# Performance work log

Hardware: AMD Instinct MI355X
Metric: run time of the kernel (lower is better)

The kernel has to match this reference:

```python
import jax, jax.numpy as jnp
import numpy as np

H = 1024      # hidden_size
NH = 16       # num heads
HD = H // NH  # head dim
B, S = 2, 2048


def setup_inputs() -> dict:
    key = jax.random.key(0)
    ks = jax.random.split(key, 10)
    s = 1.0 / np.sqrt(H)
    return {
        "hidden_states": jax.random.normal(ks[0], (B, S, H), dtype=jnp.float32),
        "attention_mask": jax.random.randint(ks[1], (B, S), 0, 2, dtype=jnp.int32),
        "Wq": jax.random.normal(ks[2], (H, H), dtype=jnp.float32) * s,
        "bq": jnp.zeros((H,), dtype=jnp.float32),
        "Wk": jax.random.normal(ks[3], (H, H), dtype=jnp.float32) * s,
        "bk": jnp.zeros((H,), dtype=jnp.float32),
        "Wv": jax.random.normal(ks[4], (H, H), dtype=jnp.float32) * s,
        "bv": jnp.zeros((H,), dtype=jnp.float32),
        "Wo": jax.random.normal(ks[5], (H, H), dtype=jnp.float32) * s,
        "bo": jnp.zeros((H,), dtype=jnp.float32),
    }


def _heads(x):
    # [B,S,H] -> [B,NH,S,HD]
    b, s, _ = x.shape
    return x.reshape(b, s, NH, HD).transpose(0, 2, 1, 3)


def reference(hidden_states, attention_mask, Wq, bq, Wk, bk, Wv, bv, Wo, bo):
    q = _heads(hidden_states @ Wq + bq)
    k = _heads(hidden_states @ Wk + bk)
    v = _heads(hidden_states @ Wv + bv)
    scores = jnp.einsum("bhqd,bhkd->bhqk", q, k) / jnp.sqrt(jnp.float32(HD))
    mask = attention_mask.astype(scores.dtype)[:, None, None, :]  # [B,1,1,S]
    scores = scores + mask * -10000.0
    probs = jax.nn.softmax(scores, axis=-1)  # dropout is identity in eval
    ctx = jnp.einsum("bhqk,bhkd->bhqd", probs, v)
    ctx = ctx.transpose(0, 2, 1, 3).reshape(hidden_states.shape[0], hidden_states.shape[1], H)
    return ctx @ Wo + bo
```

## Files before the change

kernel.cpp:

```cpp
#include <hip/hip_runtime.h>
#include <stdint.h>
#include <stddef.h>

#define S_LEN 2048
#define BATCH 2
#define HID 1024
#define NHEADS 16
#define HDIM 64

typedef __attribute__((ext_vector_type(8))) short short8;
typedef __attribute__((ext_vector_type(4))) short short4v;
typedef __attribute__((ext_vector_type(4))) float float4v;

#define MFMA32(a, b, c) __builtin_amdgcn_mfma_f32_16x16x32_bf16((a), (b), (c), 0, 0, 0)

#if __has_builtin(__builtin_amdgcn_mfma_f32_16x16x16_bf16)
#define MFMA16(a, b, c) __builtin_amdgcn_mfma_f32_16x16x16_bf16((a), (b), (c), 0, 0, 0)
#elif __has_builtin(__builtin_amdgcn_mfma_f32_16x16x16bf16_1k)
#define MFMA16(a, b, c) __builtin_amdgcn_mfma_f32_16x16x16bf16_1k((a), (b), (c), 0, 0, 0)
#else
static __device__ __forceinline__ float4v mfma16_asm(short4v a, short4v b, float4v c) {
  asm volatile("v_mfma_f32_16x16x16_bf16 %0, %1, %2, %0" : "+v"(c) : "v"(a), "v"(b));
  return c;
}
#define MFMA16(a, b, c) mfma16_asm((a), (b), (c))
#endif

#define SCALE_L2E 0.18033688011f

__device__ __forceinline__ short f2bf(float f) {
  union { float f; uint32_t u; } v; v.f = f;
  uint32_t u = v.u;
  uint32_t r = (u + 0x7fffu + ((u >> 16) & 1u)) >> 16;
  return (short)(uint16_t)r;
}

__device__ __forceinline__ short4v pack_bf16x4(float4v v) {
  union { short4v s; uint32_t u[2]; } U;
  U.u[0] = __builtin_amdgcn_perm(__float_as_uint(v[1]) + 0x8000u,
                                 __float_as_uint(v[0]) + 0x8000u, 0x07060302u);
  U.u[1] = __builtin_amdgcn_perm(__float_as_uint(v[3]) + 0x8000u,
                                 __float_as_uint(v[2]) + 0x8000u, 0x07060302u);
  return U.s;
}

__device__ __forceinline__ void gl_lds16(const void* g, void* l) {
  __builtin_amdgcn_global_load_lds((const __attribute__((address_space(1))) void*)g,
                                   (__attribute__((address_space(3))) void*)l,
                                   16, 0, 0);
}

__global__ __launch_bounds__(256) void prep_cast(const float* __restrict__ x,
                                                 const int* __restrict__ mask,
                                                 short* __restrict__ xbf,
                                                 short* __restrict__ maskb) {
  int gid = blockIdx.x * 256 + threadIdx.x;
  const float4v* src = (const float4v*)x;
  float4v v = src[gid];
  short4v o;
  o[0] = f2bf(v[0]); o[1] = f2bf(v[1]); o[2] = f2bf(v[2]); o[3] = f2bf(v[3]);
  ((short4v*)xbf)[gid] = o;
  if (gid < BATCH * S_LEN) maskb[gid] = f2bf(-14426.9504f * (float)mask[gid]);
}

__global__ __launch_bounds__(256) void prep_transpose(const float* __restrict__ w0,
                                                      const float* __restrict__ w1,
                                                      const float* __restrict__ w2,
                                                      const float* __restrict__ w3,
                                                      short* __restrict__ wt) {
  __shared__ short lds[64 * 66];
  int z = blockIdx.z;
  const float* w = (z == 0) ? w0 : (z == 1) ? w1 : (z == 2) ? w2 : w3;
  short* out = wt + (size_t)z * HID * HID;
  int k0 = blockIdx.x * 64, n0 = blockIdx.y * 64;
  int lane = threadIdx.x & 63, wrp = threadIdx.x >> 6;
#pragma unroll
  for (int i = 0; i < 16; i++) {
    int rr = wrp + i * 4;
    lds[lane * 66 + rr] = f2bf(w[(size_t)(k0 + rr) * HID + n0 + lane]);
  }
  __syncthreads();
#pragma unroll
  for (int i = 0; i < 16; i++) {
    int nn = wrp + i * 4;
    out[(size_t)(n0 + nn) * HID + k0 + lane] = lds[nn * 66 + lane];
  }
}

#define VPS 136
template <int BM, int BN, bool TRANS_EP, bool DBUF>
__global__ __launch_bounds__(256) void gemm_bt(const short* __restrict__ A,
                                               const short* __restrict__ WTbase,
                                               const float* __restrict__ bq,
                                               const float* __restrict__ bk,
                                               const float* __restrict__ bv,
                                               const float* __restrict__ bo,
                                               short* __restrict__ outQ,
                                               short* __restrict__ outK,
                                               short* __restrict__ outVt,
                                               float* __restrict__ outF,
                                               int mode_base) {
  constexpr int RI = BM / 32;
  constexpr int RJ = BN / 32;
  constexpr int TILE = BM * 128 + BN * 128;
  constexpr int LSZ1 = DBUF ? TILE * 2 : TILE;
  constexpr int LSZ = (TRANS_EP && LSZ1 < 128 * VPS * 2) ? 128 * VPS * 2 : LSZ1;
  __shared__ __align__(16) char lds[LSZ];
  const int tid = threadIdx.x;
  const int lane = tid & 63, w = tid >> 6;
  const int wm = w & 1, wn = w >> 1;
  const int quad = lane >> 4, l15 = lane & 15;
  const int mode = mode_base + blockIdx.z;
  const short* Bt = WTbase + (size_t)mode * HID * HID;
  const float* bias = (mode == 0) ? bq : (mode == 1) ? bk : (mode == 2) ? bv : bo;
  const int m0 = blockIdx.x * BM, n0 = blockIdx.y * BN;

  float4v acc[RI][RJ];
#pragma unroll
  for (int i = 0; i < RI; i++)
#pragma unroll
    for (int j = 0; j < RJ; j++) acc[i][j] = (float4v)0.0f;

  auto issue = [&](int k0, char* buf) {
#pragma unroll
    for (int inst = 0; inst < BM / 32; inst++) {
      int p = inst * 256 + tid;
      int r = p >> 3;
      int c = (p & 7) ^ (r & 7);
      gl_lds16(A + (size_t)(m0 + r) * HID + k0 + c * 8, buf + p * 16);
    }
#pragma unroll
    for (int inst = 0; inst < BN / 32; inst++) {
      int p = inst * 256 + tid;
      int r = p >> 3;
      int c = (p & 7) ^ (r & 7);
      gl_lds16(Bt + (size_t)(n0 + r) * HID + k0 + c * 8, buf + BM * 128 + p * 16);
    }
  };

  auto compute = [&](const char* buf) {
#pragma unroll
    for (int kk = 0; kk < 2; kk++) {
      short8 af[RI], bf[RJ];
#pragma unroll
      for (int i = 0; i < RI; i++) {
        int ra = wm * (BM / 2) + i * 16 + l15;
        af[i] = *(const short8*)(buf + ra * 128 + (((kk * 4 + quad) ^ (ra & 7)) * 16));
      }
#pragma unroll
      for (int j = 0; j < RJ; j++) {
        int rb = wn * (BN / 2) + j * 16 + l15;
        bf[j] = *(const short8*)(buf + BM * 128 + rb * 128 + (((kk * 4 + quad) ^ (rb & 7)) * 16));
      }
#pragma unroll
      for (int i = 0; i < RI; i++)
#pragma unroll
        for (int j = 0; j < RJ; j++)
          acc[i][j] = MFMA32(af[i], bf[j], acc[i][j]);
    }
  };

  if (DBUF) {
    constexpr int NLD = BM / 32 + BN / 32;
    issue(0, lds);
#pragma unroll 1
    for (int t = 0; t < HID / 64; t++) {
      if (t < HID / 64 - 1) {
        issue((t + 1) * 64, lds + ((t + 1) & 1) * TILE);
        asm volatile("s_waitcnt vmcnt(%0)" ::"i"(NLD) : "memory");
      } else {
        asm volatile("s_waitcnt vmcnt(0)" ::: "memory");
      }
      __builtin_amdgcn_s_barrier();
      asm volatile("" ::: "memory");
      compute(lds + (t & 1) * TILE);
      asm volatile("" ::: "memory");
      __builtin_amdgcn_s_barrier();
    }
  } else {
    for (int k0 = 0; k0 < HID; k0 += 64) {
      __syncthreads();
      issue(k0, lds);
      __syncthreads();
      compute(lds);
    }
  }

  if (TRANS_EP && mode == 2) {
    short* eb = (short*)lds;
    __syncthreads();
#pragma unroll
    for (int j = 0; j < RJ; j++) {
      int nl = wn * (BN / 2) + j * 16 + l15;
      float bsv = bias[n0 + nl];
#pragma unroll
      for (int i = 0; i < RI; i++)
#pragma unroll
        for (int r = 0; r < 4; r++) {
          int ml = wm * (BM / 2) + i * 16 + quad * 4 + r;
          eb[nl * VPS + ml] = f2bf(acc[i][j][r] + bsv);
        }
    }
    __syncthreads();
    int row = tid >> 1, half = tid & 1;
    int n = n0 + row, h = n >> 6, d = n & 63;
    int b = m0 >> 11, sc = (m0 & 2047) + half * 64;
    short* dst = outVt + ((size_t)(b * NHEADS + h) * HDIM + d) * S_LEN + sc;
    const short* src = eb + row * VPS + half * 64;
#pragma unroll
    for (int c = 0; c < 8; c++)
      *(short8*)(dst + c * 8) = *(const short8*)(src + c * 8);
    return;
  }

#pragma unroll
  for (int i = 0; i < RI; i++) {
#pragma unroll
    for (int j = 0; j < RJ; j++) {
      int n = n0 + wn * (BN / 2) + j * 16 + l15;
      float bsv = bias[n];
#pragma unroll
      for (int r = 0; r < 4; r++) {
        int m = m0 + wm * (BM / 2) + i * 16 + quad * 4 + r;
        float val = acc[i][j][r] + bsv;
        if (mode == 3) {
          outF[(size_t)m * HID + n] = val;
        } else {
          int b = m >> 11, s = m & 2047, h = n >> 6, d = n & 63;
          if (mode == 1) val *= SCALE_L2E;
          short u = f2bf(val);
          if (mode == 0)
            outQ[((size_t)(b * NHEADS + h) * S_LEN + s) * HDIM + d] = u;
          else
            outK[((size_t)(b * NHEADS + h) * S_LEN + s) * HDIM + d] = u;
        }
      }
    }
  }
}

#define AT_DB 16384
#define AT_VOFF 8192
#define ALDS_M 32768

__device__ __forceinline__ float* buf_addr(float* base, int row, int col) {
  return base + row * 64 + ((((col >> 2) ^ (row & 15)) << 2) | (col & 3));
}

__global__ __launch_bounds__(256, 4) void attn(const short* __restrict__ Qb,
                                               const short* __restrict__ Kb,
                                               const short* __restrict__ Vt,
                                               const short* __restrict__ maskb,
                                               short* __restrict__ ctx) {
  __shared__ __align__(16) char lds[36864];
  const int tid = threadIdx.x, lane = tid & 63, w = tid >> 6;
  const int quad = lane >> 4, l15 = lane & 15;
  const int qhalf = w & 1, khalf = w >> 1;
  const int h = blockIdx.y, b = blockIdx.z, bh = b * NHEADS + h;
  const short* Qh = Qb + (size_t)bh * S_LEN * HDIM;
  const short* Kh = Kb + (size_t)bh * S_LEN * HDIM;
  const short* Vh = Vt + (size_t)bh * HDIM * S_LEN;
  const short* mbase = maskb + b * S_LEN;
  const int qb0 = blockIdx.x * 64;

  auto issueKV = [&](int kb, int bufi) {
    char* base = lds + bufi * AT_DB;
#pragma unroll
    for (int inst = 0; inst < 2; inst++) {
      int p = inst * 256 + tid;
      int r = p >> 3, c = (p & 7) ^ (r & 7);
      gl_lds16(Kh + (size_t)(kb + r) * HDIM + c * 8, base + p * 16);
      gl_lds16(Vh + (size_t)r * S_LEN + kb + c * 8, base + AT_VOFF + p * 16);
    }
  };

  gl_lds16(mbase + tid * 8, lds + ALDS_M + tid * 16);
  issueKV(0, 0);

  short8 qf[2][2];
#pragma unroll
  for (int qt = 0; qt < 2; qt++)
#pragma unroll
    for (int kk = 0; kk < 2; kk++)
      qf[qt][kk] = *(const short8*)(Qh + (size_t)(qb0 + qhalf * 32 + qt * 16 + l15) * HDIM + kk * 32 + quad * 8);

  float4v o[2][4];
#pragma unroll
  for (int qt = 0; qt < 2; qt++)
#pragma unroll
    for (int nd = 0; nd < 4; nd++) o[qt][nd] = (float4v)0.0f;
  float lp[2] = {0.0f, 0.0f};

#pragma unroll 1
  for (int kb = 0; kb < S_LEN; kb += 64) {
    const int cur = (kb >> 6) & 1;
    const char* base = lds + cur * AT_DB;
    if (kb + 64 < S_LEN) {
      issueKV(kb + 64, cur ^ 1);
      asm volatile("s_waitcnt vmcnt(%0)" ::"i"(4) : "memory");
    } else {
      asm volatile("s_waitcnt vmcnt(0)" ::: "memory");
    }
    __builtin_amdgcn_s_barrier();
    asm volatile("" ::: "memory");

#pragma unroll
    for (int mt = 0; mt < 2; mt++) {
      short4v bvf[4];
      {
        int ch = khalf * 4 + mt * 2 + (quad >> 1);
        int sub = (quad & 1) * 8;
#pragma unroll
        for (int nd = 0; nd < 4; nd++) {
          int rv = nd * 16 + l15;
          bvf[nd] = *(const short4v*)(base + AT_VOFF + rv * 128 + ((ch ^ (rv & 7)) * 16) + sub);
        }
      }
      int rk = khalf * 32 + mt * 16 + l15;
      short8 ka0 = *(const short8*)(base + rk * 128 + ((quad ^ (rk & 7)) * 16));
      short8 ka1 = *(const short8*)(base + rk * 128 + (((4 + quad) ^ (rk & 7)) * 16));
      float4v mbv;
      {
        int midx = kb + khalf * 32 + mt * 16 + quad * 4;
        short4v ms = *(const short4v*)(lds + ALDS_M + midx * 2);
#pragma unroll
        for (int r = 0; r < 4; r++)
          mbv[r] = __uint_as_float(((uint32_t)(uint16_t)ms[r]) << 16);
      }
#pragma unroll
      for (int qt = 0; qt < 2; qt++) {
        float4v c = mbv;
        c = MFMA32(ka0, qf[qt][0], c);
        c = MFMA32(ka1, qf[qt][1], c);
        float4v ev;
#pragma unroll
        for (int r = 0; r < 4; r++) ev[r] = __builtin_amdgcn_exp2f(c[r]);
        lp[qt] += (ev[0] + ev[1]) + (ev[2] + ev[3]);
        short4v ap = pack_bf16x4(ev);
#pragma unroll
        for (int nd = 0; nd < 4; nd++) o[qt][nd] = MFMA16(ap, bvf[nd], o[qt][nd]);
      }
    }
    asm volatile("" ::: "memory");
    __builtin_amdgcn_s_barrier();
  }

#pragma unroll
  for (int qt = 0; qt < 2; qt++) {
    lp[qt] += __shfl_xor(lp[qt], 16, 64);
    lp[qt] += __shfl_xor(lp[qt], 32, 64);
  }
  float* lrowS = (float*)(lds + ALDS_M);
  float* bufP = (float*)(lds + qhalf * 8192);
  if (quad == 0) {
#pragma unroll
    for (int qt = 0; qt < 2; qt++) lrowS[w * 32 + qt * 16 + l15] = lp[qt];
  }
  if (khalf == 1) {
#pragma unroll
    for (int qt = 0; qt < 2; qt++)
#pragma unroll
      for (int nd = 0; nd < 4; nd++)
#pragma unroll
        for (int r = 0; r < 4; r++)
          *buf_addr(bufP, qt * 16 + quad * 4 + r, nd * 16 + l15) = o[qt][nd][r];
  }
  __syncthreads();
  if (khalf == 0) {
#pragma unroll
    for (int qt = 0; qt < 2; qt++)
#pragma unroll
      for (int nd = 0; nd < 4; nd++)
#pragma unroll
        for (int r = 0; r < 4; r++) {
          float* p = buf_addr(bufP, qt * 16 + quad * 4 + r, nd * 16 + l15);
          *p = *p + o[qt][nd][r];
        }
  }
  __syncthreads();
  int row = w * 16 + l15;
  float ls = lrowS[row] + lrowS[64 + row];
  float inv = 1.0f / ls;
  float* bufq = (float*)(lds + (row >> 5) * 8192);
  int brow = row & 31;
  short* dstp = ctx + ((size_t)(b * S_LEN + qb0 + row) * HID + h * HDIM + quad * 16);
#pragma unroll
  for (int half = 0; half < 2; half++) {
    int c0 = quad * 16 + half * 8;
    float4v x0 = *(float4v*)buf_addr(bufq, brow, c0);
    float4v x1 = *(float4v*)buf_addr(bufq, brow, c0 + 4);
    union { short8 s; short4v h[2]; } R;
    float4v s0, s1;
#pragma unroll
    for (int i = 0; i < 4; i++) { s0[i] = x0[i] * inv; s1[i] = x1[i] * inv; }
    R.h[0] = pack_bf16x4(s0);
    R.h[1] = pack_bf16x4(s1);
    *(short8*)(dstp + half * 8) = R.s;
  }
}

extern "C" void kernel_launch(void* const* d_in, const int* in_sizes, int n_in,
                              void* d_out, int out_size, void* d_ws, size_t ws_size,
                              hipStream_t stream) {
  const float* hs = (const float*)d_in[0];
  const int* mask = (const int*)d_in[1];
  const float* Wq = (const float*)d_in[2];
  const float* bq = (const float*)d_in[3];
  const float* Wk = (const float*)d_in[4];
  const float* bk = (const float*)d_in[5];
  const float* Wv = (const float*)d_in[6];
  const float* bv = (const float*)d_in[7];
  const float* Wo = (const float*)d_in[8];
  const float* bo = (const float*)d_in[9];
  float* out = (float*)d_out;
  char* ws = (char*)d_ws;

  short* XBF = (short*)(ws);
  short* CTX = (short*)(ws);
  short* WT  = (short*)(ws + (size_t)(8u << 20));
  short* QB  = (short*)(ws + (size_t)(16u << 20));
  short* KB  = (short*)(ws + (size_t)(24u << 20));
  short* VTt = (short*)(ws + (size_t)(32u << 20));
  short* MB  = (short*)(ws + (size_t)(40u << 20));

  prep_cast<<<4096, 256, 0, stream>>>(hs, mask, XBF, MB);
  prep_transpose<<<dim3(16, 16, 4), 256, 0, stream>>>(Wq, Wk, Wv, Wo, WT);
  gemm_bt<128, 128, true, true><<<dim3(32, 8, 3), 256, 0, stream>>>(XBF, WT, bq, bk, bv, bo, QB, KB, VTt, nullptr, 0);
  attn<<<dim3(32, NHEADS, BATCH), 256, 0, stream>>>(QB, KB, VTt, MB, CTX);
  gemm_bt<64, 128, false, true><<<dim3(64, 8, 1), 256, 0, stream>>>(CTX, WT, bq, bk, bv, bo, nullptr, nullptr, nullptr, out, 3);
}
```

Before: 192.0 us.

## Compact unmasked keys so attention skips masked key blocks

Adds a single-block prep kernel that prefix-sums the attention mask into a compacted key index, a padded key count per batch, and a compacted additive mask. The QKV GEMM epilogue scatters K and transposed V rows into compacted positions, and the attention loop runs only over the padded count of unmasked keys. The goal is to skip roughly the fraction of key blocks whose softmax weight is negligible. In exchange, the V epilogue switches from vectorized stores to per-element scattered stores, and a fully masked batch row would give a zero-length loop instead of the reference's uniform softmax.

```diff
diff --git a/kernel.cpp b/kernel.cpp
--- a/kernel.cpp
+++ b/kernel.cpp
@@ -51,16 +51,67 @@
 }
 
 __global__ __launch_bounds__(256) void prep_cast(const float* __restrict__ x,
-                                                 const int* __restrict__ mask,
-                                                 short* __restrict__ xbf,
-                                                 short* __restrict__ maskb) {
+                                                 short* __restrict__ xbf) {
   int gid = blockIdx.x * 256 + threadIdx.x;
   const float4v* src = (const float4v*)x;
   float4v v = src[gid];
   short4v o;
   o[0] = f2bf(v[0]); o[1] = f2bf(v[1]); o[2] = f2bf(v[2]); o[3] = f2bf(v[3]);
   ((short4v*)xbf)[gid] = o;
-  if (gid < BATCH * S_LEN) maskb[gid] = f2bf(-14426.9504f * (float)mask[gid]);
+}
+
+__global__ __launch_bounds__(256) void prep_idx(const int* __restrict__ mask,
+                                                short* __restrict__ maskc,
+                                                short* __restrict__ cidx,
+                                                int* __restrict__ nkinfo,
+                                                short* __restrict__ Kc,
+                                                short* __restrict__ Vtc) {
+  __shared__ int sc[256];
+  const int t = threadIdx.x;
+  const short neg = f2bf(-14426.9504f);
+  for (int b = 0; b < BATCH; b++) {
+    int m[8]; int lc = 0;
+    const int* mb = mask + b * S_LEN + t * 8;
+#pragma unroll
+    for (int j = 0; j < 8; j++) { m[j] = mb[j]; lc += (m[j] == 0); }
+    sc[t] = lc;
+    __syncthreads();
+#pragma unroll
+    for (int off = 1; off < 256; off <<= 1) {
+      int u = (t >= off) ? sc[t - off] : 0;
+      int v = sc[t];
+      __syncthreads();
+      sc[t] = u + v;
+      __syncthreads();
+    }
+    int excl = sc[t] - lc;
+    int nk = sc[255];
+    int nkpad = (nk + 63) & ~63;
+    if (t == 0) nkinfo[b] = nkpad;
+    int run = excl;
+#pragma unroll
+    for (int j = 0; j < 8; j++) {
+      short v;
+      if (m[j] == 0) { v = (short)run; maskc[b * S_LEN + run] = 0; run++; }
+      else v = (short)-1;
+      cidx[b * S_LEN + t * 8 + j] = v;
+    }
+    for (int i = nk + t; i < S_LEN; i += 256) maskc[b * S_LEN + i] = neg;
+    for (int p = t; p < NHEADS * 64; p += 256) {
+      int hh = p >> 6, sp = nk + (p & 63);
+      if (sp < nkpad) {
+        short* dst = Kc + ((size_t)(b * NHEADS + hh) * S_LEN + sp) * HDIM;
+#pragma unroll
+        for (int c8 = 0; c8 < 8; c8++) *(short8*)(dst + c8 * 8) = (short8)0;
+      }
+    }
+    for (int p = t; p < NHEADS * HDIM; p += 256) {
+      int hh = p >> 6, dd = p & 63;
+      short* dst = Vtc + ((size_t)(b * NHEADS + hh) * HDIM + dd) * S_LEN;
+      for (int sp = nk; sp < nkpad; sp++) dst[sp] = 0;
+    }
+    __syncthreads();
+  }
 }
 
 __global__ __launch_bounds__(256) void prep_transpose(const float* __restrict__ w0,
@@ -99,6 +150,7 @@
                                                short* __restrict__ outK,
                                                short* __restrict__ outVt,
                                                float* __restrict__ outF,
+                                               const short* __restrict__ cidx,
                                                int mode_base) {
   constexpr int RI = BM / 32;
   constexpr int RJ = BN / 32;
@@ -204,12 +256,15 @@
     __syncthreads();
     int row = tid >> 1, half = tid & 1;
     int n = n0 + row, h = n >> 6, d = n & 63;
-    int b = m0 >> 11, sc = (m0 & 2047) + half * 64;
-    short* dst = outVt + ((size_t)(b * NHEADS + h) * HDIM + d) * S_LEN + sc;
+    int b = m0 >> 11;
+    short* dsth = outVt + ((size_t)(b * NHEADS + h) * HDIM + d) * S_LEN;
     const short* src = eb + row * VPS + half * 64;
-#pragma unroll
-    for (int c = 0; c < 8; c++)
-      *(short8*)(dst + c * 8) = *(const short8*)(src + c * 8);
+    const short* cb = cidx + b * S_LEN + (m0 & 2047) + half * 64;
+#pragma unroll 8
+    for (int j = 0; j < 64; j++) {
+      int sp = cb[j];
+      if (sp >= 0) dsth[sp] = src[j];
+    }
     return;
   }
 
@@ -227,12 +282,14 @@
           outF[(size_t)m * HID + n] = val;
         } else {
           int b = m >> 11, s = m & 2047, h = n >> 6, d = n & 63;
-          if (mode == 1) val *= SCALE_L2E;
-          short u = f2bf(val);
-          if (mode == 0)
+          short u = f2bf((mode == 1) ? val * SCALE_L2E : val);
+          if (mode == 0) {
             outQ[((size_t)(b * NHEADS + h) * S_LEN + s) * HDIM + d] = u;
-          else
-            outK[((size_t)(b * NHEADS + h) * S_LEN + s) * HDIM + d] = u;
+          } else {
+            int sp = cidx[b * S_LEN + s];
+            if (sp >= 0)
+              outK[((size_t)(b * NHEADS + h) * S_LEN + sp) * HDIM + d] = u;
+          }
         }
       }
     }
@@ -250,7 +307,8 @@
 __global__ __launch_bounds__(256, 4) void attn(const short* __restrict__ Qb,
                                                const short* __restrict__ Kb,
                                                const short* __restrict__ Vt,
-                                               const short* __restrict__ maskb,
+                                               const short* __restrict__ maskc,
+                                               const int* __restrict__ nkinfo,
                                                short* __restrict__ ctx) {
   __shared__ __align__(16) char lds[36864];
   const int tid = threadIdx.x, lane = tid & 63, w = tid >> 6;
@@ -260,8 +318,9 @@
   const short* Qh = Qb + (size_t)bh * S_LEN * HDIM;
   const short* Kh = Kb + (size_t)bh * S_LEN * HDIM;
   const short* Vh = Vt + (size_t)bh * HDIM * S_LEN;
-  const short* mbase = maskb + b * S_LEN;
+  const short* mbase = maskc + b * S_LEN;
   const int qb0 = blockIdx.x * 64;
+  const int nkp = nkinfo[b];
 
   auto issueKV = [&](int kb, int bufi) {
     char* base = lds + bufi * AT_DB;
@@ -292,10 +351,10 @@
   float lp[2] = {0.0f, 0.0f};
 
 #pragma unroll 1
-  for (int kb = 0; kb < S_LEN; kb += 64) {
+  for (int kb = 0; kb < nkp; kb += 64) {
     const int cur = (kb >> 6) & 1;
     const char* base = lds + cur * AT_DB;
-    if (kb + 64 < S_LEN) {
+    if (kb + 64 < nkp) {
       issueKV(kb + 64, cur ^ 1);
       asm volatile("s_waitcnt vmcnt(%0)" ::"i"(4) : "memory");
     } else {
@@ -421,11 +480,14 @@
   short* QB  = (short*)(ws + (size_t)(16u << 20));
   short* KB  = (short*)(ws + (size_t)(24u << 20));
   short* VTt = (short*)(ws + (size_t)(32u << 20));
-  short* MB  = (short*)(ws + (size_t)(40u << 20));
-
-  prep_cast<<<4096, 256, 0, stream>>>(hs, mask, XBF, MB);
+  short* MBc = (short*)(ws + (size_t)(40u << 20));
+  short* CIDX = (short*)(ws + (size_t)(40u << 20) + (64u << 10));
+  int*   NKI  = (int*)(ws + (size_t)(40u << 20) + (128u << 10));
+
+  prep_cast<<<4096, 256, 0, stream>>>(hs, XBF);
+  prep_idx<<<1, 256, 0, stream>>>(mask, MBc, CIDX, NKI, KB, VTt);
   prep_transpose<<<dim3(16, 16, 4), 256, 0, stream>>>(Wq, Wk, Wv, Wo, WT);
-  gemm_bt<128, 128, true, true><<<dim3(32, 8, 3), 256, 0, stream>>>(XBF, WT, bq, bk, bv, bo, QB, KB, VTt, nullptr, 0);
-  attn<<<dim3(32, NHEADS, BATCH), 256, 0, stream>>>(QB, KB, VTt, MB, CTX);
-  gemm_bt<64, 128, false, true><<<dim3(64, 8, 1), 256, 0, stream>>>(CTX, WT, bq, bk, bv, bo, nullptr, nullptr, nullptr, out, 3);
-}
+  gemm_bt<128, 128, true, true><<<dim3(32, 8, 3), 256, 0, stream>>>(XBF, WT, bq, bk, bv, bo, QB, KB, VTt, nullptr, CIDX, 0);
+  attn<<<dim3(32, NHEADS, BATCH), 256, 0, stream>>>(QB, KB, VTt, MBc, NKI, CTX);
+  gemm_bt<64, 128, false, true><<<dim3(64, 8, 1), 256, 0, stream>>>(CTX, WT, bq, bk, bv, bo, nullptr, nullptr, nullptr, out, nullptr, 3);
+}
```

Measured after the change: 200.2 us. +4.3%, slower.
